# Optimization experiments

Measured on AMD Instinct MI355X. Metric: run time of the kernel, lower is better.

Reference implementation:

```python
import jax, jax.numpy as jnp
import numpy as np

T, N, NL, H, COND, NE, NSI, VOCAB = 32, 256, 16, 256, 64, 8, 16, 64


def _gru_step(h, x, wih, whh, bih, bhh):
    gi = x @ wih.T + bih
    gh = h @ whh.T + bhh
    ir, iz, inn = jnp.split(gi, 3, axis=-1)
    hr, hz, hn = jnp.split(gh, 3, axis=-1)
    r = jax.nn.sigmoid(ir + hr)
    z = jax.nn.sigmoid(iz + hz)
    n = jnp.tanh(inn + r * hn)
    return (1.0 - z) * n + z * h


def _run_gru(xs, wih, whh, bih, bhh, reverse=False):
    # xs: [B, L, D] -> [B, L, H]; zero initial state (torch default)
    def step(h, x):
        h = _gru_step(h, x, wih, whh, bih, bhh)
        return h, h
    h0 = jnp.zeros((xs.shape[0], whh.shape[1]), xs.dtype)
    _, ys = jax.lax.scan(step, h0, jnp.swapaxes(xs, 0, 1), reverse=reverse)
    return jnp.swapaxes(ys, 0, 1)


def _forward(condition, lines, actions, h0, w0, embed,
             gwih_f, gwhh_f, gbih_f, gbhh_f, gwih_b, gwhh_b, gbih_b, gbhh_b,
             w2, b2, cwih, cwhh, cbih, cbhh, mw1, mb1, mw2, mb2,
             ow, ob, aw, ab, cw, cb):
    M = embed[lines]                                   # [N, NL, H]
    # rolled[i] = roll(M, -i, axis=1); cat along batch dim -> [NL*N, NL, H]
    idx = (jnp.arange(NL)[:, None] + jnp.arange(NL)[None, :]) % NL
    rolled = jnp.transpose(M[:, idx], (1, 0, 2, 3)).reshape(NL * N, NL, H)
    yf = _run_gru(rolled, gwih_f, gwhh_f, gbih_f, gbhh_f)
    yb = _run_gru(rolled, gwih_b, gwhh_b, gbih_b, gbhh_b, reverse=True)
    G = jnp.stack([yf, yb], axis=2).reshape(NL, N, NL, 2, H)
    # pointer construction (no_scan=False branch)
    B = jax.nn.sigmoid(jnp.einsum('injdh,eh->injde', G, w2) + b2)  # [NL,N,NL,2,NE]
    f, b = B[..., 0, :], B[..., 1, :]
    Bc = jnp.stack([f, b[:, :, ::-1]], axis=3).reshape(NL, N, 2 * NL, NE)
    zero_last = Bc.at[:, :, -1].set(0.0)
    B2 = zero_last.at[:, :, -1].set(1.0)
    C = jnp.cumprod(1.0 - jnp.roll(zero_last, 1, axis=2), axis=2)
    P = (B2 * C).reshape(NL, N, NL, 2, NE)
    f2, b2p = P[..., 0, :], P[..., 1, :]
    P = jnp.concatenate([b2p[:, :, ::-1], f2], axis=2)  # [NL, N, 2NL, NE]
    P = jnp.roll(P, (-1, 1), axis=(0, 2))
    # per-timestep recurrence
    Rn = jnp.arange(N)
    A_seq = actions[:, :, 0]
    W_seq = actions[:, :, 1]

    def step(carry, xs):
        h, w = carry
        cond_t, A_t, W_t = xs
        x = jnp.concatenate([cond_t, M[Rn, w]], axis=-1)
        h = _gru_step(h, x, cwih, cwhh, cbih, cbhh)
        z = jax.nn.relu(jax.nn.relu(jax.nn.relu(h @ mw1.T + mb1) @ mw2.T + mb2))
        a_probs = jax.nn.softmax(z @ aw.T + ab)          # [N, NSI]
        o = jax.nn.softmax(z @ ow.T + ob)                # [N, NE]
        g = P[w, Rn]                                     # [N, 2NL, NE]
        p_probs = jnp.einsum('nke,ne->nk', g, o)         # [N, 2NL]
        v = z @ cw.T + cb                                # [N, 1]
        w_new = jnp.clip(w + W_t - NL, 0, NL - 1)
        fdt = z.dtype
        out = jnp.concatenate([
            A_t[:, None].astype(fdt), W_t[:, None].astype(fdt),
            w_new[:, None].astype(fdt), v, h, a_probs, p_probs], axis=-1)
        return (h, w_new), out

    _, ys = jax.lax.scan(step, (h0, w0), (condition, A_seq, W_seq))
    return ys  # [T, N, 4 + H + NSI + 2*NL]


def setup_inputs() -> dict:
    key = jax.random.key(0)
    ks = jax.random.split(key, 40)
    rn = lambda i, shape, s=0.05: (jax.random.normal(ks[i], shape) * s).astype(jnp.float32)
    H3 = 3 * H
    inp = {
        'condition': jax.random.normal(ks[0], (T, N, COND), jnp.float32),
        'lines': jax.random.randint(ks[1], (N, NL), 0, VOCAB, jnp.int32),
        'actions': jax.random.randint(ks[2], (T, N, 2), 0, 8, jnp.int32),
        'h0': jnp.zeros((N, H), jnp.float32),
        'w0': jnp.zeros((N,), jnp.int32),
        'embed': rn(3, (VOCAB, H), 0.5),
        'gwih_f': rn(4, (H3, H)), 'gwhh_f': rn(5, (H3, H)),
        'gbih_f': rn(6, (H3,)), 'gbhh_f': rn(7, (H3,)),
        'gwih_b': rn(8, (H3, H)), 'gwhh_b': rn(9, (H3, H)),
        'gbih_b': rn(10, (H3,)), 'gbhh_b': rn(11, (H3,)),
        'w2': rn(12, (NE, H)), 'b2': rn(13, (NE,)),
        'cwih': rn(14, (H3, H + COND)), 'cwhh': rn(15, (H3, H)),
        'cbih': rn(16, (H3,)), 'cbhh': rn(17, (H3,)),
        'mw1': rn(18, (H, H)), 'mb1': rn(19, (H,)),
        'mw2': rn(20, (H, H)), 'mb2': rn(21, (H,)),
        'ow': rn(22, (NE, H)), 'ob': rn(23, (NE,)),
        'aw': rn(24, (NSI, H)), 'ab': rn(25, (NSI,)),
        'cw': rn(26, (1, H)), 'cb': rn(27, (1,)),
    }
    return inp


def reference(condition, lines, actions, h0, w0, embed,
              gwih_f, gwhh_f, gbih_f, gbhh_f, gwih_b, gwhh_b, gbih_b, gbhh_b,
              w2, b2, cwih, cwhh, cbih, cbhh, mw1, mb1, mw2, mb2,
              ow, ob, aw, ab, cw, cb):
    return _forward(condition, lines, actions, h0, w0, embed,
                    gwih_f, gwhh_f, gbih_f, gbhh_f, gwih_b, gwhh_b, gbih_b, gbhh_b,
                    w2, b2, cwih, cwhh, cbih, cbhh, mw1, mb1, mw2, mb2,
                    ow, ob, aw, ab, cw, cb)
```

## Files before the change

### kernel.cpp

```cpp
#include <hip/hip_runtime.h>
#include <cstddef>
#include <cstdint>

#define TT   32
#define NN   256
#define NLL  16
#define HH   256
#define CONDD 64
#define NEE  8
#define H3   768
#define OW   308

typedef __attribute__((ext_vector_type(8))) short bf16x8;
typedef __attribute__((ext_vector_type(4))) float f32x4;
typedef unsigned short u16;

__device__ __forceinline__ float sigm(float x)     { return 1.f / (1.f + __expf(-x)); }
__device__ __forceinline__ float tanhfast(float x) { return 1.f - 2.f / (__expf(2.f * x) + 1.f); }
__device__ __forceinline__ float bf2f(u16 h) {
    union { unsigned u; float f; } v; v.u = ((unsigned)h) << 16; return v.f;
}
__device__ __forceinline__ u16 f2bf(float f) {
    union { float f; unsigned u; } v; v.f = f;
    unsigned r = v.u + 0x7fffu + ((v.u >> 16) & 1u);
    return (u16)(r >> 16);
}
#define MFMA(a, b, c) __builtin_amdgcn_mfma_f32_16x16x32_bf16(a, b, c, 0, 0, 0)

__device__ __forceinline__ void gl_lds16(const u16* g, u16* l) {
    __builtin_amdgcn_global_load_lds(
        (const __attribute__((address_space(1))) unsigned int*)(const void*)g,
        (__attribute__((address_space(3))) unsigned int*)(void*)l, 16, 0, 0);
}
__device__ __forceinline__ void stage_chunk(const u16* __restrict__ W, u16* buf,
                                            int c, int w, int lane) {
#pragma unroll
    for (int r = 0; r < 8; ++r) {
        int gran = (w * 8 + r) * 64 + lane;
        int cic = gran >> 5, gs = gran & 31;
        const u16* src = W + ((size_t)(c * 128 + cic) << 8) + ((gs ^ (cic & 7)) << 3);
        gl_lds16(src, buf + ((w * 8 + r) << 9));
    }
}
__device__ __forceinline__ void wait_vm8()   { asm volatile("s_waitcnt vmcnt(8)" ::: "memory"); }
__device__ __forceinline__ void wait_vm0()   { asm volatile("s_waitcnt vmcnt(0)" ::: "memory"); }
__device__ __forceinline__ void wait_lgkm0() { asm volatile("s_waitcnt lgkmcnt(0)" ::: "memory"); }
__device__ __forceinline__ void bar() {
    asm volatile("" ::: "memory");
    __builtin_amdgcn_s_barrier();
    asm volatile("" ::: "memory");
}

__global__ __launch_bounds__(256) void k_prep(
    const float* __restrict__ gwhh_f, const float* __restrict__ gwhh_b,
    const float* __restrict__ cwhh,  const float* __restrict__ mw1,
    const float* __restrict__ mw2,   const float* __restrict__ condition,
    const float* __restrict__ cwih,
    u16* __restrict__ whhbf_f, u16* __restrict__ whhbf_b, u16* __restrict__ cwhhbf,
    u16* __restrict__ mw1bf, u16* __restrict__ mw2bf, u16* __restrict__ condbf,
    u16* __restrict__ cwcbf)
{
    long i = (long)blockIdx.x * 256 + threadIdx.x;
    if (i < 196608) { whhbf_f[i] = f2bf(gwhh_f[i]); return; } i -= 196608;
    if (i < 196608) { whhbf_b[i] = f2bf(gwhh_b[i]); return; } i -= 196608;
    if (i < 196608) { cwhhbf[i]  = f2bf(cwhh[i]);  return; } i -= 196608;
    if (i < 65536)  { mw1bf[i]   = f2bf(mw1[i]);   return; } i -= 65536;
    if (i < 65536)  { mw2bf[i]   = f2bf(mw2[i]);   return; } i -= 65536;
    if (i < 524288) { condbf[i]  = f2bf(condition[i]); return; } i -= 524288;
    if (i < 49152)  { long r = i >> 6, c = i & 63; cwcbf[i] = f2bf(cwih[r * 320 + c]); }
}

__global__ __launch_bounds__(256) void k_tok_gi(
    const float* __restrict__ embed,
    const float* __restrict__ gwih_f, const float* __restrict__ gbih_f,
    const float* __restrict__ gwih_b, const float* __restrict__ gbih_b,
    const float* __restrict__ cwih,   const float* __restrict__ cbih,
    u16* __restrict__ gif, u16* __restrict__ gib, u16* __restrict__ gic)
{
    int v = blockIdx.x, tid = threadIdx.x;
    __shared__ float es[256];
    es[tid] = embed[v * HH + tid];
    __syncthreads();
    for (int g = 0; g < 3; ++g) {
        int col = g * 256 + tid;
        float af = gbih_f[col], abv = gbih_b[col], ac = cbih[col];
        const float* wf = gwih_f + (size_t)col * HH;
        const float* wb = gwih_b + (size_t)col * HH;
        const float* wc = cwih   + (size_t)col * (HH + CONDD) + CONDD;
        for (int c = 0; c < 256; ++c) {
            float e = es[c];
            af += e * wf[c]; abv += e * wb[c]; ac += e * wc[c];
        }
        gif[v * H3 + col] = f2bf(af);
        gib[v * H3 + col] = f2bf(abv);
        gic[v * H3 + col] = f2bf(ac);
    }
}

__global__ void k_wtraj(const int* __restrict__ actions, const int* __restrict__ w0,
                        const int* __restrict__ lines,
                        float* __restrict__ out, int* __restrict__ w_used,
                        int* __restrict__ tok_used)
{
    int n = threadIdx.x;
    int w = w0[n];
    for (int t = 0; t < TT; ++t) {
        int A = actions[((size_t)t * NN + n) * 2 + 0];
        int W = actions[((size_t)t * NN + n) * 2 + 1];
        w_used[t * NN + n] = w;
        tok_used[t * NN + n] = lines[n * NLL + w];
        int wn = w + W - NLL;
        wn = wn < 0 ? 0 : (wn > NLL - 1 ? NLL - 1 : wn);
        float* o = out + ((size_t)t * NN + n) * OW;
        o[0] = (float)A; o[1] = (float)W; o[2] = (float)wn;
        w = wn;
    }
}

__global__ __launch_bounds__(512) void k_gru(
    const u16* __restrict__ whhbf_f, const u16* __restrict__ whhbf_b,
    const u16* __restrict__ gif, const u16* __restrict__ gib,
    const float* __restrict__ gbhh_f, const float* __restrict__ gbhh_b,
    const float* __restrict__ w2, const float* __restrict__ b2,
    float* __restrict__ Bf, float* __restrict__ Bb,
    const int* __restrict__ lines)
{
    __shared__ __align__(16) u16 hbf[32 * 264];
    __shared__ __align__(16) u16 wbuf[2][32768];
    __shared__ float w2s[8 * 256];
    __shared__ int   lns[32 * 16];

    const int tid = threadIdx.x, lane = tid & 63, w = tid >> 6;
    const int lm = lane & 15, lg = lane >> 4;
    const int bid = blockIdx.x, dir = bid >> 7, lb = bid & 127;
    const int ii = lb >> 3, nb = (lb & 7) * 32;
    const u16*   whh  = dir ? whhbf_b : whhbf_f;
    const u16*   git  = dir ? gib : gif;
    const float* bhh  = dir ? gbhh_b : gbhh_f;
    float*       Bout = dir ? Bb : Bf;

    const int cicw = w * 16 + lm;
    const int cc0 = cicw, cc1 = cicw + 128;
    const float b_r[2] = { bhh[cc0],       bhh[cc1] };
    const float b_z[2] = { bhh[cc0 + 256], bhh[cc1 + 256] };
    const float b_n[2] = { bhh[cc0 + 512], bhh[cc1 + 512] };
    const float b2e = b2[tid & 7];

    for (int k = tid; k < 32 * 264; k += 512) hbf[k] = 0;
    for (int k = tid; k < 2048; k += 512) w2s[k] = w2[k];
    lns[tid & 511] = lines[(nb + (tid >> 4)) * NLL + (tid & 15)];
    __syncthreads();

    stage_chunk(whh, wbuf[0], 0, w, lane);

    for (int s = 0; s < 16; ++s) {
        const int jpos = dir ? (15 - s) : s;
        const int jt = (ii + jpos) & 15;

        bf16x8 a[2][8];
        #pragma unroll
        for (int ks = 0; ks < 8; ++ks) {
            a[0][ks] = *(const bf16x8*)&hbf[lm * 264 + ks * 32 + lg * 8];
            a[1][ks] = *(const bf16x8*)&hbf[(16 + lm) * 264 + ks * 32 + lg * 8];
        }
        f32x4 acc[6][2];
        #pragma unroll
        for (int c = 0; c < 6; ++c)
            #pragma unroll
            for (int rf = 0; rf < 2; ++rf)
                #pragma unroll
                for (int z = 0; z < 4; ++z) acc[c][rf][z] = 0.f;

        #pragma unroll
        for (int c = 0; c < 6; ++c) {
            if (s == 15 && c == 5) { wait_vm0(); }
            else { stage_chunk(whh, wbuf[(c + 1) & 1], (c + 1) % 6, w, lane); wait_vm8(); }
            bar();
            const u16* wb = wbuf[c & 1];
            #pragma unroll
            for (int ks = 0; ks < 8; ++ks) {
                bf16x8 b = *(const bf16x8*)&wb[(size_t)cicw * 256 + (((ks * 4 + lg) ^ (lm & 7)) << 3)];
                acc[c][0] = MFMA(a[0][ks], b, acc[c][0]);
                acc[c][1] = MFMA(a[1][ks], b, acc[c][1]);
            }
            bar();
        }

        float hnew[2][2][4];
        #pragma unroll
        for (int half = 0; half < 2; ++half) {
            const int cc = half ? cc1 : cc0;
            #pragma unroll
            for (int rf = 0; rf < 2; ++rf)
                #pragma unroll
                for (int j = 0; j < 4; ++j) {
                    int lrow = rf * 16 + lg * 4 + j;
                    int tok  = lns[lrow * 16 + jt];
                    const u16* gi = git + (size_t)tok * H3;
                    float ho = bf2f(hbf[lrow * 264 + cc]);
                    float rg = sigm(bf2f(gi[cc])       + acc[half][rf][j]     + b_r[half]);
                    float zg = sigm(bf2f(gi[cc + 256]) + acc[2 + half][rf][j] + b_z[half]);
                    float ng = tanhfast(bf2f(gi[cc + 512]) + rg * (acc[4 + half][rf][j] + b_n[half]));
                    hnew[half][rf][j] = (1.f - zg) * ng + zg * ho;
                }
        }
        #pragma unroll
        for (int half = 0; half < 2; ++half) {
            const int cc = half ? cc1 : cc0;
            #pragma unroll
            for (int rf = 0; rf < 2; ++rf)
                #pragma unroll
                for (int j = 0; j < 4; ++j)
                    hbf[(rf * 16 + lg * 4 + j) * 264 + cc] = f2bf(hnew[half][rf][j]);
        }
        wait_lgkm0(); bar();

        if (tid < 256) {
            int r = tid >> 3, e = tid & 7;
            float acb = b2e;
            for (int cx = 0; cx < 256; ++cx)
                acb += bf2f(hbf[r * 264 + cx]) * w2s[e * 256 + cx];
            int grow = ii * 256 + nb + r;
            Bout[((size_t)grow * NLL + jpos) * NEE + e] = sigm(acb);
        }
    }
}

__global__ __launch_bounds__(512) void k_ctrl(
    const u16* __restrict__ cwhhbf, const u16* __restrict__ cwcbf,
    const u16* __restrict__ condbf, const u16* __restrict__ gic,
    const float* __restrict__ cbhh, const float* __restrict__ h0,
    const int* __restrict__ tok_used,
    u16* __restrict__ Hallbf, float* __restrict__ out)
{
    __shared__ __align__(16) u16 hc[16 * 264];
    __shared__ __align__(16) u16 wbuf[2][32768];
    __shared__ int toks[16];

    const int tid = threadIdx.x, lane = tid & 63, w = tid >> 6;
    const int lm = lane & 15, lg = lane >> 4;
    const int cb = blockIdx.x;
    const int cicw = w * 16 + lm;
    const int cc0 = cicw, cc1 = cicw + 128;

    bf16x8 wc[6][2];
    #pragma unroll
    for (int c = 0; c < 6; ++c)
        #pragma unroll
        for (int k2 = 0; k2 < 2; ++k2)
            wc[c][k2] = *(const bf16x8*)&cwcbf[(size_t)(c * 128 + cicw) * 64 + k2 * 32 + lg * 8];

    const float cb_r[2] = { cbhh[cc0],       cbhh[cc1] };
    const float cb_z[2] = { cbhh[cc0 + 256], cbhh[cc1 + 256] };
    const float cb_n[2] = { cbhh[cc0 + 512], cbhh[cc1 + 512] };

    if (tid < 256) {
        int lrow = tid >> 4, c0 = (tid & 15) * 16;
        u16 tmp[16];
        #pragma unroll
        for (int k = 0; k < 16; ++k)
            tmp[k] = f2bf(h0[(size_t)(cb * 16 + lrow) * HH + c0 + k]);
        *(uint4*)&hc[lrow * 264 + c0]     = *(uint4*)&tmp[0];
        *(uint4*)&hc[lrow * 264 + c0 + 8] = *(uint4*)&tmp[8];
    }
    __syncthreads();

    stage_chunk(cwhhbf, wbuf[0], 0, w, lane);

    for (int t = 0; t < TT; ++t) {
        if (tid < 16) toks[tid] = tok_used[t * NN + cb * 16 + tid];

        bf16x8 a[8];
        #pragma unroll
        for (int ks = 0; ks < 8; ++ks)
            a[ks] = *(const bf16x8*)&hc[lm * 264 + ks * 32 + lg * 8];
        bf16x8 ca[2];
        #pragma unroll
        for (int k2 = 0; k2 < 2; ++k2)
            ca[k2] = *(const bf16x8*)&condbf[(size_t)(t * NN + cb * 16 + lm) * 64 + k2 * 32 + lg * 8];

        f32x4 acc[6], accC[2];
        #pragma unroll
        for (int c = 0; c < 6; ++c)
            #pragma unroll
            for (int z = 0; z < 4; ++z) acc[c][z] = 0.f;
        #pragma unroll
        for (int c = 0; c < 2; ++c)
            #pragma unroll
            for (int z = 0; z < 4; ++z) accC[c][z] = 0.f;

        #pragma unroll
        for (int c = 0; c < 6; ++c)
            #pragma unroll
            for (int k2 = 0; k2 < 2; ++k2) {
                if (c < 4) acc[c]      = MFMA(ca[k2], wc[c][k2], acc[c]);
                else       accC[c - 4] = MFMA(ca[k2], wc[c][k2], accC[c - 4]);
            }

        #pragma unroll
        for (int c = 0; c < 6; ++c) {
            if (t == 31 && c == 5) { wait_vm0(); }
            else { stage_chunk(cwhhbf, wbuf[(c + 1) & 1], (c + 1) % 6, w, lane); wait_vm8(); }
            bar();
            const u16* wb = wbuf[c & 1];
            #pragma unroll
            for (int ks = 0; ks < 8; ++ks) {
                bf16x8 b = *(const bf16x8*)&wb[(size_t)cicw * 256 + (((ks * 4 + lg) ^ (lm & 7)) << 3)];
                acc[c] = MFMA(a[ks], b, acc[c]);
            }
            bar();
        }

        float hn2[2][4];
        #pragma unroll
        for (int half = 0; half < 2; ++half) {
            const int cc = half ? cc1 : cc0;
            #pragma unroll
            for (int j = 0; j < 4; ++j) {
                int lrow = lg * 4 + j;
                int n = cb * 16 + lrow;
                int tok = toks[lrow];
                const u16* gi = gic + (size_t)tok * H3;
                float ho = bf2f(hc[lrow * 264 + cc]);
                float rg = sigm(bf2f(gi[cc])       + acc[half][j]     + cb_r[half]);
                float zg = sigm(bf2f(gi[cc + 256]) + acc[2 + half][j] + cb_z[half]);
                float ng = tanhfast(bf2f(gi[cc + 512]) + accC[half][j]
                                    + rg * (acc[4 + half][j] + cb_n[half]));
                float hn = (1.f - zg) * ng + zg * ho;
                out[((size_t)t * NN + n) * OW + 4 + cc] = hn;
                Hallbf[((size_t)t * NN + n) * HH + cc] = f2bf(hn);
                hn2[half][j] = hn;
            }
        }
        #pragma unroll
        for (int half = 0; half < 2; ++half) {
            const int cc = half ? cc1 : cc0;
            #pragma unroll
            for (int j = 0; j < 4; ++j)
                hc[(lg * 4 + j) * 264 + cc] = f2bf(hn2[half][j]);
        }
        wait_lgkm0(); bar();
    }
}

__global__ __launch_bounds__(256) void k_stick(
    const float* __restrict__ Bf, const float* __restrict__ Bb,
    float* __restrict__ P_final)
{
    int idx = blockIdx.x * 256 + threadIdx.x;
    if (idx >= 16 * 256 * 8) return;
    int e = idx & 7, n = (idx >> 3) & 255, i = idx >> 11;
    const float* bf = Bf + ((size_t)(i * NN + n) * NLL) * NEE + e;
    const float* bb = Bb + ((size_t)(i * NN + n) * NLL) * NEE + e;
    int i2 = (i + 15) & 15;
    float* dst = P_final + ((size_t)(i2 * NN + n) * 32) * NEE + e;
    float cum = 1.f;
    #pragma unroll
    for (int m = 0; m < 16; ++m) {
        float c0 = bf[m * NEE];
        float c1 = bb[(15 - m) * NEE];
        float v0 = c0 * cum;
        cum *= (1.f - c0);
        float v1 = (m < 15) ? c1 * cum : cum;
        cum *= (1.f - c1);
        dst[(size_t)(((17 + m) & 31)) * NEE] = v0;
        dst[(size_t)((16 - m)) * NEE]        = v1;
    }
}

__global__ __launch_bounds__(256) void k_mlp(
    const u16* __restrict__ A, const u16* __restrict__ W,
    const float* __restrict__ bias, u16* __restrict__ Out)
{
    __shared__ u16 ot[32 * 264];
    const int g0 = blockIdx.x * 32;
    const int tid = threadIdx.x, lane = tid & 63, w = tid >> 6;
    const int lm = lane & 15, lg = lane >> 4;
    f32x4 acc[4][2];
    #pragma unroll
    for (int c = 0; c < 4; ++c)
        #pragma unroll
        for (int r = 0; r < 2; ++r)
            #pragma unroll
            for (int z = 0; z < 4; ++z) acc[c][r][z] = 0.f;
    #pragma unroll
    for (int ks = 0; ks < 8; ++ks) {
        bf16x8 a0 = *(const bf16x8*)&A[(size_t)(g0 + lm) * 256 + ks * 32 + lg * 8];
        bf16x8 a1 = *(const bf16x8*)&A[(size_t)(g0 + 16 + lm) * 256 + ks * 32 + lg * 8];
        #pragma unroll
        for (int cf = 0; cf < 4; ++cf) {
            const u16* bp = W + (size_t)(w * 64 + cf * 16 + lm) * 256 + ks * 32 + lg * 8;
            bf16x8 b = *(const bf16x8*)bp;
            acc[cf][0] = MFMA(a0, b, acc[cf][0]);
            acc[cf][1] = MFMA(a1, b, acc[cf][1]);
        }
    }
    #pragma unroll
    for (int cf = 0; cf < 4; ++cf) {
        int col = w * 64 + cf * 16 + lm;
        float bs = bias[col];
        #pragma unroll
        for (int rf = 0; rf < 2; ++rf)
            #pragma unroll
            for (int j = 0; j < 4; ++j) {
                int lrow = rf * 16 + lg * 4 + j;
                ot[lrow * 264 + col] = f2bf(fmaxf(acc[cf][rf][j] + bs, 0.f));
            }
    }
    __syncthreads();
    int lrow = tid >> 3, c0 = (tid & 7) * 32;
    const uint4* src = (const uint4*)&ot[lrow * 264 + c0];
    uint4* dst = (uint4*)&Out[(size_t)(g0 + lrow) * 256 + c0];
    dst[0] = src[0]; dst[1] = src[1]; dst[2] = src[2]; dst[3] = src[3];
}

__global__ __launch_bounds__(256) void k_heads(
    const u16* __restrict__ zbf,
    const float* __restrict__ aw, const float* __restrict__ ab,
    const float* __restrict__ ow, const float* __restrict__ ob,
    const float* __restrict__ cw, const float* __restrict__ cb,
    const float* __restrict__ P_final, const int* __restrict__ w_used,
    float* __restrict__ out)
{
    __shared__ float zt[32 * 258];
    __shared__ float hd[32][28];
    __shared__ float o8[32][8];
    __shared__ int   wv[32];
    const int g0 = blockIdx.x * 32, tid = threadIdx.x;
    {
        int lrow = tid >> 3, c0 = (tid & 7) * 32;
        const u16* src = &zbf[(size_t)(g0 + lrow) * 256 + c0];
        #pragma unroll
        for (int k = 0; k < 32; ++k) zt[lrow * 258 + c0 + k] = bf2f(src[k]);
    }
    if (tid < 32) wv[tid] = w_used[g0 + tid];
    __syncthreads();
    {
        int r = tid >> 3, s = tid & 7;
        const float* z = &zt[r * 258];
        float a1 = ab[s], a2 = ab[8 + s], a3 = ob[s], a4 = cb[0];
        const float* w1 = aw + s * 256;
        const float* w2_ = aw + (8 + s) * 256;
        const float* w3 = ow + s * 256;
        for (int c = 0; c < 256; ++c) {
            float zv = z[c];
            a1 += zv * w1[c]; a2 += zv * w2_[c]; a3 += zv * w3[c]; a4 += zv * cw[c];
        }
        hd[r][s] = a1; hd[r][8 + s] = a2; hd[r][16 + s] = a3;
        if (s == 0) hd[r][24] = a4;
    }
    __syncthreads();
    if (tid < 32) {
        int r = tid; int g = g0 + r;
        float* orow = out + (size_t)g * OW;
        float mx = hd[r][0];
        #pragma unroll
        for (int k = 1; k < 16; ++k) mx = fmaxf(mx, hd[r][k]);
        float ex[16], ssum = 0.f;
        #pragma unroll
        for (int k = 0; k < 16; ++k) { ex[k] = __expf(hd[r][k] - mx); ssum += ex[k]; }
        float inv = 1.f / ssum;
        #pragma unroll
        for (int k = 0; k < 16; ++k) orow[260 + k] = ex[k] * inv;
        orow[3] = hd[r][24];
        float mo = hd[r][16];
        #pragma unroll
        for (int k = 1; k < 8; ++k) mo = fmaxf(mo, hd[r][16 + k]);
        float eo[8], so = 0.f;
        #pragma unroll
        for (int k = 0; k < 8; ++k) { eo[k] = __expf(hd[r][16 + k] - mo); so += eo[k]; }
        float invo = 1.f / so;
        #pragma unroll
        for (int k = 0; k < 8; ++k) o8[r][k] = eo[k] * invo;
    }
    __syncthreads();
    {
        int r = tid >> 3, kb = tid & 7;
        int g = g0 + r, n = g & 255;
        const float* base = P_final + ((size_t)(wv[r] * NN + n) * 32) * NEE;
        float* orow = out + (size_t)g * OW + 276;
        #pragma unroll
        for (int m = 0; m < 4; ++m) {
            int k = kb + m * 8;
            const float* pe = base + k * NEE;
            float a = 0.f;
            #pragma unroll
            for (int e = 0; e < 8; ++e) a += pe[e] * o8[r][e];
            orow[k] = a;
        }
    }
}

extern "C" void kernel_launch(void* const* d_in, const int* in_sizes, int n_in,
                              void* d_out, int out_size, void* d_ws, size_t ws_size,
                              hipStream_t stream) {
    const float* condition = (const float*)d_in[0];
    const int*   lines     = (const int*)  d_in[1];
    const int*   actions   = (const int*)  d_in[2];
    const float* h0        = (const float*)d_in[3];
    const int*   w0        = (const int*)  d_in[4];
    const float* embed     = (const float*)d_in[5];
    const float* gwih_f    = (const float*)d_in[6];
    const float* gwhh_f    = (const float*)d_in[7];
    const float* gbih_f    = (const float*)d_in[8];
    const float* gbhh_f    = (const float*)d_in[9];
    const float* gwih_b    = (const float*)d_in[10];
    const float* gwhh_b    = (const float*)d_in[11];
    const float* gbih_b    = (const float*)d_in[12];
    const float* gbhh_b    = (const float*)d_in[13];
    const float* w2        = (const float*)d_in[14];
    const float* b2        = (const float*)d_in[15];
    const float* cwih      = (const float*)d_in[16];
    const float* cwhh      = (const float*)d_in[17];
    const float* cbih      = (const float*)d_in[18];
    const float* cbhh      = (const float*)d_in[19];
    const float* mw1       = (const float*)d_in[20];
    const float* mb1       = (const float*)d_in[21];
    const float* mw2       = (const float*)d_in[22];
    const float* mb2       = (const float*)d_in[23];
    const float* ow        = (const float*)d_in[24];
    const float* ob        = (const float*)d_in[25];
    const float* aw        = (const float*)d_in[26];
    const float* ab        = (const float*)d_in[27];
    const float* cw        = (const float*)d_in[28];
    const float* cb        = (const float*)d_in[29];
    float* out = (float*)d_out;

    char* base = (char*)d_ws;
    auto alloc = [&](size_t bytes) { char* r = base; base += (bytes + 255) & ~(size_t)255; return r; };
    u16*   gif_tok = (u16*)alloc(64 * H3 * 2);
    u16*   gib_tok = (u16*)alloc(64 * H3 * 2);
    u16*   gic_tok = (u16*)alloc(64 * H3 * 2);
    u16*   whhbf_f = (u16*)alloc(H3 * 256 * 2);
    u16*   whhbf_b = (u16*)alloc(H3 * 256 * 2);
    u16*   cwhhbf  = (u16*)alloc(H3 * 256 * 2);
    u16*   mw1bf   = (u16*)alloc(256 * 256 * 2);
    u16*   mw2bf   = (u16*)alloc(256 * 256 * 2);
    u16*   cwcbf   = (u16*)alloc(H3 * 64 * 2);
    u16*   condbf  = (u16*)alloc((size_t)TT * NN * CONDD * 2);
    float* Bf      = (float*)alloc((size_t)16 * 256 * 16 * 8 * 4);
    float* Bb      = (float*)alloc((size_t)16 * 256 * 16 * 8 * 4);
    float* P_final = (float*)alloc((size_t)16 * 256 * 32 * 8 * 4);
    u16*   Hallbf  = (u16*)alloc((size_t)TT * NN * 256 * 2);
    u16*   zbf     = (u16*)alloc((size_t)TT * NN * 256 * 2);
    int*   w_used  = (int*)alloc((size_t)TT * NN * 4);
    int*   tok_used= (int*)alloc((size_t)TT * NN * 4);
    u16*   z1bf    = (u16*)Bf;

    k_prep<<<5056, 256, 0, stream>>>(gwhh_f, gwhh_b, cwhh, mw1, mw2, condition, cwih,
                                     whhbf_f, whhbf_b, cwhhbf, mw1bf, mw2bf, condbf, cwcbf);

    k_tok_gi<<<64, 256, 0, stream>>>(embed, gwih_f, gbih_f, gwih_b, gbih_b, cwih, cbih,
                                     gif_tok, gib_tok, gic_tok);
    k_wtraj<<<1, 256, 0, stream>>>(actions, w0, lines, out, w_used, tok_used);

    k_gru<<<256, 512, 0, stream>>>(whhbf_f, whhbf_b, gif_tok, gib_tok, gbhh_f, gbhh_b,
                                   w2, b2, Bf, Bb, lines);

    k_ctrl<<<16, 512, 0, stream>>>(cwhhbf, cwcbf, condbf, gic_tok, cbhh, h0, tok_used,
                                   Hallbf, out);

    k_stick<<<128, 256, 0, stream>>>(Bf, Bb, P_final);

    k_mlp<<<256, 256, 0, stream>>>(Hallbf, mw1bf, mb1, z1bf);
    k_mlp<<<256, 256, 0, stream>>>(z1bf, mw2bf, mb2, zbf);

    k_heads<<<256, 256, 0, stream>>>(zbf, aw, ab, ow, ob, cw, cb, P_final, w_used, out);
}
```

Before: 727.1 us.

## Merge pointer GRU and controller GRU into one concurrent kernel with 64-row tiles

Fuses the bidirectional pointer GRU and the controller GRU into a single launch. Blocks 0-127 run the pointer scans over 64 rows each, and blocks 128-131 run the controller over 64 rows each, so the long serial controller chain overlaps with the pointer work. The condition projection is precomputed for all timesteps by a new MFMA kernel into a gi_full buffer, and the token input projections and the r/z recurrent biases are folded together with MFMA. The w2 head now uses MFMA instead of a scalar loop, and hidden state is carried in fp32 registers. The costs are a large extra gi_full intermediate, buffer aliasing, and only 4 controller blocks, each doing a 32-step chain over more rows per step.

```diff
diff --git a/kernel.cpp b/kernel.cpp
--- a/kernel.cpp
+++ b/kernel.cpp
@@ -25,6 +25,12 @@
     unsigned r = v.u + 0x7fffu + ((v.u >> 16) & 1u);
     return (u16)(r >> 16);
 }
+__device__ __forceinline__ bf16x8 pack8(float4 f0, float4 f1) {
+    union { u16 u[8]; bf16x8 v; } r;
+    r.u[0] = f2bf(f0.x); r.u[1] = f2bf(f0.y); r.u[2] = f2bf(f0.z); r.u[3] = f2bf(f0.w);
+    r.u[4] = f2bf(f1.x); r.u[5] = f2bf(f1.y); r.u[6] = f2bf(f1.z); r.u[7] = f2bf(f1.w);
+    return r.v;
+}
 #define MFMA(a, b, c) __builtin_amdgcn_mfma_f32_16x16x32_bf16(a, b, c, 0, 0, 0)
 
 __device__ __forceinline__ void gl_lds16(const u16* g, u16* l) {
@@ -32,17 +38,17 @@
         (const __attribute__((address_space(1))) unsigned int*)(const void*)g,
         (__attribute__((address_space(3))) unsigned int*)(void*)l, 16, 0, 0);
 }
-__device__ __forceinline__ void stage_chunk(const u16* __restrict__ W, u16* buf,
-                                            int c, int w, int lane) {
+__device__ __forceinline__ void stage96(const u16* __restrict__ W, u16* buf,
+                                        int c, int w, int lane) {
 #pragma unroll
-    for (int r = 0; r < 8; ++r) {
-        int gran = (w * 8 + r) * 64 + lane;
-        int cic = gran >> 5, gs = gran & 31;
-        const u16* src = W + ((size_t)(c * 128 + cic) << 8) + ((gs ^ (cic & 7)) << 3);
-        gl_lds16(src, buf + ((w * 8 + r) << 9));
-    }
-}
-__device__ __forceinline__ void wait_vm8()   { asm volatile("s_waitcnt vmcnt(8)" ::: "memory"); }
+    for (int r = 0; r < 6; ++r) {
+        int gran = (w * 6 + r) * 64 + lane;
+        int row  = gran >> 5, gs = gran & 31;
+        const u16* src = W + ((size_t)(c * 96 + row) << 8) + ((gs ^ (row & 7)) << 3);
+        gl_lds16(src, buf + ((w * 6 + r) << 9));
+    }
+}
+__device__ __forceinline__ void wait_vm6()   { asm volatile("s_waitcnt vmcnt(6)" ::: "memory"); }
 __device__ __forceinline__ void wait_vm0()   { asm volatile("s_waitcnt vmcnt(0)" ::: "memory"); }
 __device__ __forceinline__ void wait_lgkm0() { asm volatile("s_waitcnt lgkmcnt(0)" ::: "memory"); }
 __device__ __forceinline__ void bar() {
@@ -54,10 +60,10 @@
 __global__ __launch_bounds__(256) void k_prep(
     const float* __restrict__ gwhh_f, const float* __restrict__ gwhh_b,
     const float* __restrict__ cwhh,  const float* __restrict__ mw1,
-    const float* __restrict__ mw2,   const float* __restrict__ condition,
+    const float* __restrict__ mw2,   const float* __restrict__ w2,
     const float* __restrict__ cwih,
     u16* __restrict__ whhbf_f, u16* __restrict__ whhbf_b, u16* __restrict__ cwhhbf,
-    u16* __restrict__ mw1bf, u16* __restrict__ mw2bf, u16* __restrict__ condbf,
+    u16* __restrict__ mw1bf, u16* __restrict__ mw2bf, u16* __restrict__ w2bf,
     u16* __restrict__ cwcbf)
 {
     long i = (long)blockIdx.x * 256 + threadIdx.x;
@@ -66,34 +72,58 @@
     if (i < 196608) { cwhhbf[i]  = f2bf(cwhh[i]);  return; } i -= 196608;
     if (i < 65536)  { mw1bf[i]   = f2bf(mw1[i]);   return; } i -= 65536;
     if (i < 65536)  { mw2bf[i]   = f2bf(mw2[i]);   return; } i -= 65536;
-    if (i < 524288) { condbf[i]  = f2bf(condition[i]); return; } i -= 524288;
+    if (i < 4096)   { long r = i >> 8, c = i & 255;
+                      w2bf[i] = (r < 8) ? f2bf(w2[r * 256 + c]) : (u16)0; return; } i -= 4096;
     if (i < 49152)  { long r = i >> 6, c = i & 63; cwcbf[i] = f2bf(cwih[r * 320 + c]); }
 }
 
-__global__ __launch_bounds__(256) void k_tok_gi(
+__global__ __launch_bounds__(256) void k_tok(
     const float* __restrict__ embed,
-    const float* __restrict__ gwih_f, const float* __restrict__ gbih_f,
-    const float* __restrict__ gwih_b, const float* __restrict__ gbih_b,
-    const float* __restrict__ cwih,   const float* __restrict__ cbih,
+    const float* __restrict__ gwih_f, const float* __restrict__ gbih_f, const float* __restrict__ gbhh_f,
+    const float* __restrict__ gwih_b, const float* __restrict__ gbih_b, const float* __restrict__ gbhh_b,
+    const float* __restrict__ cwih,   const float* __restrict__ cbih,   const float* __restrict__ cbhh,
     u16* __restrict__ gif, u16* __restrict__ gib, u16* __restrict__ gic)
 {
-    int v = blockIdx.x, tid = threadIdx.x;
-    __shared__ float es[256];
-    es[tid] = embed[v * HH + tid];
-    __syncthreads();
-    for (int g = 0; g < 3; ++g) {
-        int col = g * 256 + tid;
-        float af = gbih_f[col], abv = gbih_b[col], ac = cbih[col];
-        const float* wf = gwih_f + (size_t)col * HH;
-        const float* wb = gwih_b + (size_t)col * HH;
-        const float* wc = cwih   + (size_t)col * (HH + CONDD) + CONDD;
-        for (int c = 0; c < 256; ++c) {
-            float e = es[c];
-            af += e * wf[c]; abv += e * wb[c]; ac += e * wc[c];
-        }
-        gif[v * H3 + col] = f2bf(af);
-        gib[v * H3 + col] = f2bf(abv);
-        gic[v * H3 + col] = f2bf(ac);
+    const int mat = blockIdx.x / 6, ch = blockIdx.x % 6;
+    const int tid = threadIdx.x, lane = tid & 63, w = tid >> 6;
+    const int lm = lane & 15, lg = lane >> 4;
+    const float *W, *b1, *b2v; int wstride, woff; u16* dst;
+    if (mat == 0)      { W = gwih_f; b1 = gbih_f; b2v = gbhh_f; wstride = 256; woff = 0;  dst = gif; }
+    else if (mat == 1) { W = gwih_b; b1 = gbih_b; b2v = gbhh_b; wstride = 256; woff = 0;  dst = gib; }
+    else               { W = cwih;   b1 = cbih;   b2v = cbhh;   wstride = 320; woff = 64; dst = gic; }
+
+    bf16x8 a[8];
+    #pragma unroll
+    for (int ks = 0; ks < 8; ++ks) {
+        const float* ep = embed + (size_t)(w * 16 + lm) * 256 + ks * 32 + lg * 8;
+        a[ks] = pack8(*(const float4*)ep, *(const float4*)(ep + 4));
+    }
+    f32x4 acc[8];
+    #pragma unroll
+    for (int nt = 0; nt < 8; ++nt)
+        #pragma unroll
+        for (int z = 0; z < 4; ++z) acc[nt][z] = 0.f;
+
+    #pragma unroll
+    for (int nt = 0; nt < 8; ++nt) {
+        int col = ch * 128 + nt * 16 + lm;
+        const float* wp = W + (size_t)col * wstride + woff;
+        #pragma unroll
+        for (int ks = 0; ks < 8; ++ks) {
+            bf16x8 b = pack8(*(const float4*)(wp + ks * 32 + lg * 8),
+                             *(const float4*)(wp + ks * 32 + lg * 8 + 4));
+            acc[nt] = MFMA(a[ks], b, acc[nt]);
+        }
+    }
+    #pragma unroll
+    for (int nt = 0; nt < 8; ++nt) {
+        int col = ch * 128 + nt * 16 + lm;
+        float bias = b1[col] + (col < 512 ? b2v[col] : 0.f);
+        #pragma unroll
+        for (int j = 0; j < 4; ++j) {
+            int v = w * 16 + lg * 4 + j;
+            dst[(size_t)v * H3 + col] = f2bf(acc[nt][j] + bias);
+        }
     }
 }
 
@@ -117,229 +147,214 @@
     }
 }
 
-__global__ __launch_bounds__(512) void k_gru(
+__global__ __launch_bounds__(256) void k_cg(
+    const float* __restrict__ condition, const u16* __restrict__ cwcbf,
+    const u16* __restrict__ gic, const int* __restrict__ tok_used,
+    u16* __restrict__ gi_full)
+{
+    const int r0 = blockIdx.x * 32;
+    const int tid = threadIdx.x, lane = tid & 63, w = tid >> 6;
+    const int wm = w >> 1, wn = w & 1;
+    const int lm = lane & 15, lg = lane >> 4;
+
+    bf16x8 a[2];
+    #pragma unroll
+    for (int ks = 0; ks < 2; ++ks) {
+        const float* cp = condition + (size_t)(r0 + wm * 16 + lm) * 64 + ks * 32 + lg * 8;
+        a[ks] = pack8(*(const float4*)cp, *(const float4*)(cp + 4));
+    }
+    f32x4 acc[24];
+    #pragma unroll
+    for (int jj = 0; jj < 24; ++jj)
+        #pragma unroll
+        for (int z = 0; z < 4; ++z) acc[jj][z] = 0.f;
+
+    #pragma unroll
+    for (int jj = 0; jj < 24; ++jj) {
+        int tile = 2 * jj + wn;
+        const u16* bp = cwcbf + (size_t)(tile * 16 + lm) * 64;
+        #pragma unroll
+        for (int ks = 0; ks < 2; ++ks)
+            acc[jj] = MFMA(a[ks], *(const bf16x8*)(bp + ks * 32 + lg * 8), acc[jj]);
+    }
+    int wv[4];
+    #pragma unroll
+    for (int j = 0; j < 4; ++j) wv[j] = tok_used[r0 + wm * 16 + lg * 4 + j];
+    #pragma unroll
+    for (int jj = 0; jj < 24; ++jj) {
+        int col = (2 * jj + wn) * 16 + lm;
+        #pragma unroll
+        for (int j = 0; j < 4; ++j) {
+            int g = r0 + wm * 16 + lg * 4 + j;
+            float v = acc[jj][j] + bf2f(gic[(size_t)wv[j] * H3 + col]);
+            gi_full[(size_t)g * H3 + col] = f2bf(v);
+        }
+    }
+}
+
+__global__ __launch_bounds__(512) void k_mega(
     const u16* __restrict__ whhbf_f, const u16* __restrict__ whhbf_b,
+    const u16* __restrict__ cwhhbf,
     const u16* __restrict__ gif, const u16* __restrict__ gib,
     const float* __restrict__ gbhh_f, const float* __restrict__ gbhh_b,
-    const float* __restrict__ w2, const float* __restrict__ b2,
+    const float* __restrict__ cbhh,
+    const u16* __restrict__ w2bf, const float* __restrict__ b2,
     float* __restrict__ Bf, float* __restrict__ Bb,
-    const int* __restrict__ lines)
-{
-    __shared__ __align__(16) u16 hbf[32 * 264];
-    __shared__ __align__(16) u16 wbuf[2][32768];
-    __shared__ float w2s[8 * 256];
-    __shared__ int   lns[32 * 16];
+    const int* __restrict__ lines,
+    const u16* __restrict__ gi_full, const float* __restrict__ h0,
+    u16* __restrict__ Hallbf, float* __restrict__ out)
+{
+    __shared__ __align__(16) u16 hlds[64 * 264];
+    __shared__ __align__(16) u16 wbuf[2][96 * 256];
+    __shared__ __align__(16) u16 w2l[4096];
+    __shared__ int lns[1024];
 
     const int tid = threadIdx.x, lane = tid & 63, w = tid >> 6;
     const int lm = lane & 15, lg = lane >> 4;
-    const int bid = blockIdx.x, dir = bid >> 7, lb = bid & 127;
-    const int ii = lb >> 3, nb = (lb & 7) * 32;
-    const u16*   whh  = dir ? whhbf_b : whhbf_f;
-    const u16*   git  = dir ? gib : gif;
-    const float* bhh  = dir ? gbhh_b : gbhh_f;
-    float*       Bout = dir ? Bb : Bf;
-
-    const int cicw = w * 16 + lm;
-    const int cc0 = cicw, cc1 = cicw + 128;
-    const float b_r[2] = { bhh[cc0],       bhh[cc1] };
-    const float b_z[2] = { bhh[cc0 + 256], bhh[cc1 + 256] };
-    const float b_n[2] = { bhh[cc0 + 512], bhh[cc1 + 512] };
-    const float b2e = b2[tid & 7];
-
-    for (int k = tid; k < 32 * 264; k += 512) hbf[k] = 0;
-    for (int k = tid; k < 2048; k += 512) w2s[k] = w2[k];
-    lns[tid & 511] = lines[(nb + (tid >> 4)) * NLL + (tid & 15)];
+    const int wm = w >> 1, wn = w & 1;
+    const int bid = blockIdx.x;
+    const bool isctrl = (bid >= 128);
+
+    int dir = 0, ii = 0, nb = 0, cb = 0;
+    const u16* W; const u16* git = nullptr; const float* bnsrc;
+    float* Bout = nullptr;
+    if (isctrl) {
+        cb = bid - 128;
+        W = cwhhbf; bnsrc = cbhh;
+    } else {
+        dir = bid >> 6; int lb = bid & 63;
+        ii = lb >> 2; nb = (lb & 3) << 6;
+        W    = dir ? whhbf_b : whhbf_f;
+        git  = dir ? gib : gif;
+        bnsrc = dir ? gbhh_b : gbhh_f;
+        Bout = dir ? Bb : Bf;
+    }
+    const int smax = isctrl ? TT : 16;
+
+    float bn[8];
+    #pragma unroll
+    for (int jr = 0; jr < 8; ++jr) bn[jr] = bnsrc[512 + (2 * jr + wn) * 16 + lm];
+    const float b2e = (lm < 8) ? b2[lm] : 0.f;
+
+    float hreg[32];
+    if (isctrl) {
+        #pragma unroll
+        for (int jr = 0; jr < 8; ++jr) {
+            int col = (2 * jr + wn) * 16 + lm;
+            #pragma unroll
+            for (int j = 0; j < 4; ++j) {
+                int lrow = wm * 16 + lg * 4 + j;
+                float hv = h0[(size_t)(cb * 64 + lrow) * HH + col];
+                hreg[jr * 4 + j] = hv;
+                hlds[lrow * 264 + col] = f2bf(hv);
+            }
+        }
+    } else {
+        for (int k = tid; k < 64 * 264; k += 512) hlds[k] = 0;
+        #pragma unroll
+        for (int k = 0; k < 32; ++k) hreg[k] = 0.f;
+        for (int k = tid; k < 1024; k += 512)
+            lns[k] = lines[(nb + (k >> 4)) * NLL + (k & 15)];
+        for (int k = tid; k < 4096; k += 512) w2l[k] = w2bf[k];
+    }
     __syncthreads();
 
-    stage_chunk(whh, wbuf[0], 0, w, lane);
-
-    for (int s = 0; s < 16; ++s) {
-        const int jpos = dir ? (15 - s) : s;
-        const int jt = (ii + jpos) & 15;
-
-        bf16x8 a[2][8];
-        #pragma unroll
-        for (int ks = 0; ks < 8; ++ks) {
-            a[0][ks] = *(const bf16x8*)&hbf[lm * 264 + ks * 32 + lg * 8];
-            a[1][ks] = *(const bf16x8*)&hbf[(16 + lm) * 264 + ks * 32 + lg * 8];
-        }
-        f32x4 acc[6][2];
-        #pragma unroll
-        for (int c = 0; c < 6; ++c)
-            #pragma unroll
-            for (int rf = 0; rf < 2; ++rf)
-                #pragma unroll
-                for (int z = 0; z < 4; ++z) acc[c][rf][z] = 0.f;
-
-        #pragma unroll
-        for (int c = 0; c < 6; ++c) {
-            if (s == 15 && c == 5) { wait_vm0(); }
-            else { stage_chunk(whh, wbuf[(c + 1) & 1], (c + 1) % 6, w, lane); wait_vm8(); }
+    bf16x8 a[8];
+    #pragma unroll
+    for (int ks = 0; ks < 8; ++ks)
+        a[ks] = *(const bf16x8*)&hlds[(wm * 16 + lm) * 264 + ks * 32 + lg * 8];
+
+    stage96(W, wbuf[0], 0, w, lane);
+
+    for (int s = 0; s < smax; ++s) {
+        f32x4 acc[24];
+        #pragma unroll
+        for (int jj = 0; jj < 24; ++jj)
+            #pragma unroll
+            for (int z = 0; z < 4; ++z) acc[jj][z] = 0.f;
+
+        #pragma unroll
+        for (int c = 0; c < 8; ++c) {
+            if (c == 7 && s == smax - 1) { wait_vm0(); }
+            else { stage96(W, wbuf[(c + 1) & 1], (c + 1) & 7, w, lane); wait_vm6(); }
             bar();
             const u16* wb = wbuf[c & 1];
             #pragma unroll
-            for (int ks = 0; ks < 8; ++ks) {
-                bf16x8 b = *(const bf16x8*)&wb[(size_t)cicw * 256 + (((ks * 4 + lg) ^ (lm & 7)) << 3)];
-                acc[c][0] = MFMA(a[0][ks], b, acc[c][0]);
-                acc[c][1] = MFMA(a[1][ks], b, acc[c][1]);
+            for (int p = 0; p < 3; ++p) {
+                const int lt = wn + 2 * p;
+                const u16* bp = wb + ((lt * 16 + lm) << 8);
+                #pragma unroll
+                for (int ks = 0; ks < 8; ++ks) {
+                    bf16x8 b = *(const bf16x8*)(bp + (((ks * 4 + lg) ^ (lm & 7)) << 3));
+                    acc[c * 3 + p] = MFMA(a[ks], b, acc[c * 3 + p]);
+                }
             }
             bar();
         }
 
-        float hnew[2][2][4];
-        #pragma unroll
-        for (int half = 0; half < 2; ++half) {
-            const int cc = half ? cc1 : cc0;
-            #pragma unroll
-            for (int rf = 0; rf < 2; ++rf)
+        if (isctrl) {
+            #pragma unroll
+            for (int jr = 0; jr < 8; ++jr) {
+                const int col = (2 * jr + wn) * 16 + lm;
                 #pragma unroll
                 for (int j = 0; j < 4; ++j) {
-                    int lrow = rf * 16 + lg * 4 + j;
-                    int tok  = lns[lrow * 16 + jt];
+                    const int lrow = wm * 16 + lg * 4 + j;
+                    const size_t g = (size_t)s * NN + cb * 64 + lrow;
+                    const u16* gi = gi_full + g * H3;
+                    float rg = sigm(bf2f(gi[col])       + acc[jr][j]);
+                    float zg = sigm(bf2f(gi[col + 256]) + acc[8 + jr][j]);
+                    float ng = tanhfast(bf2f(gi[col + 512]) + rg * (acc[16 + jr][j] + bn[jr]));
+                    float hv = (1.f - zg) * ng + zg * hreg[jr * 4 + j];
+                    hreg[jr * 4 + j] = hv;
+                    hlds[lrow * 264 + col] = f2bf(hv);
+                    out[g * OW + 4 + col] = hv;
+                    Hallbf[g * HH + col] = f2bf(hv);
+                }
+            }
+        } else {
+            const int jpos = dir ? (15 - s) : s;
+            const int jt = (ii + jpos) & 15;
+            #pragma unroll
+            for (int jr = 0; jr < 8; ++jr) {
+                const int col = (2 * jr + wn) * 16 + lm;
+                #pragma unroll
+                for (int j = 0; j < 4; ++j) {
+                    const int lrow = wm * 16 + lg * 4 + j;
+                    const int tok = lns[lrow * 16 + jt];
                     const u16* gi = git + (size_t)tok * H3;
-                    float ho = bf2f(hbf[lrow * 264 + cc]);
-                    float rg = sigm(bf2f(gi[cc])       + acc[half][rf][j]     + b_r[half]);
-                    float zg = sigm(bf2f(gi[cc + 256]) + acc[2 + half][rf][j] + b_z[half]);
-                    float ng = tanhfast(bf2f(gi[cc + 512]) + rg * (acc[4 + half][rf][j] + b_n[half]));
-                    hnew[half][rf][j] = (1.f - zg) * ng + zg * ho;
+                    float rg = sigm(bf2f(gi[col])       + acc[jr][j]);
+                    float zg = sigm(bf2f(gi[col + 256]) + acc[8 + jr][j]);
+                    float ng = tanhfast(bf2f(gi[col + 512]) + rg * (acc[16 + jr][j] + bn[jr]));
+                    float hv = (1.f - zg) * ng + zg * hreg[jr * 4 + j];
+                    hreg[jr * 4 + j] = hv;
+                    hlds[lrow * 264 + col] = f2bf(hv);
                 }
-        }
-        #pragma unroll
-        for (int half = 0; half < 2; ++half) {
-            const int cc = half ? cc1 : cc0;
-            #pragma unroll
-            for (int rf = 0; rf < 2; ++rf)
+            }
+        }
+        wait_lgkm0(); bar();
+
+        #pragma unroll
+        for (int ks = 0; ks < 8; ++ks)
+            a[ks] = *(const bf16x8*)&hlds[(wm * 16 + lm) * 264 + ks * 32 + lg * 8];
+
+        if (!isctrl) {
+            const int jpos = dir ? (15 - s) : s;
+            f32x4 accB;
+            #pragma unroll
+            for (int z = 0; z < 4; ++z) accB[z] = 0.f;
+            #pragma unroll
+            for (int ks = 0; ks < 8; ++ks) {
+                bf16x8 wf = *(const bf16x8*)&w2l[lm * 256 + ks * 32 + lg * 8];
+                accB = MFMA(a[ks], wf, accB);
+            }
+            if (lm < 8) {
                 #pragma unroll
-                for (int j = 0; j < 4; ++j)
-                    hbf[(rf * 16 + lg * 4 + j) * 264 + cc] = f2bf(hnew[half][rf][j]);
-        }
-        wait_lgkm0(); bar();
-
-        if (tid < 256) {
-            int r = tid >> 3, e = tid & 7;
-            float acb = b2e;
-            for (int cx = 0; cx < 256; ++cx)
-                acb += bf2f(hbf[r * 264 + cx]) * w2s[e * 256 + cx];
-            int grow = ii * 256 + nb + r;
-            Bout[((size_t)grow * NLL + jpos) * NEE + e] = sigm(acb);
-        }
-    }
-}
-
-__global__ __launch_bounds__(512) void k_ctrl(
-    const u16* __restrict__ cwhhbf, const u16* __restrict__ cwcbf,
-    const u16* __restrict__ condbf, const u16* __restrict__ gic,
-    const float* __restrict__ cbhh, const float* __restrict__ h0,
-    const int* __restrict__ tok_used,
-    u16* __restrict__ Hallbf, float* __restrict__ out)
-{
-    __shared__ __align__(16) u16 hc[16 * 264];
-    __shared__ __align__(16) u16 wbuf[2][32768];
-    __shared__ int toks[16];
-
-    const int tid = threadIdx.x, lane = tid & 63, w = tid >> 6;
-    const int lm = lane & 15, lg = lane >> 4;
-    const int cb = blockIdx.x;
-    const int cicw = w * 16 + lm;
-    const int cc0 = cicw, cc1 = cicw + 128;
-
-    bf16x8 wc[6][2];
-    #pragma unroll
-    for (int c = 0; c < 6; ++c)
-        #pragma unroll
-        for (int k2 = 0; k2 < 2; ++k2)
-            wc[c][k2] = *(const bf16x8*)&cwcbf[(size_t)(c * 128 + cicw) * 64 + k2 * 32 + lg * 8];
-
-    const float cb_r[2] = { cbhh[cc0],       cbhh[cc1] };
-    const float cb_z[2] = { cbhh[cc0 + 256], cbhh[cc1 + 256] };
-    const float cb_n[2] = { cbhh[cc0 + 512], cbhh[cc1 + 512] };
-
-    if (tid < 256) {
-        int lrow = tid >> 4, c0 = (tid & 15) * 16;
-        u16 tmp[16];
-        #pragma unroll
-        for (int k = 0; k < 16; ++k)
-            tmp[k] = f2bf(h0[(size_t)(cb * 16 + lrow) * HH + c0 + k]);
-        *(uint4*)&hc[lrow * 264 + c0]     = *(uint4*)&tmp[0];
-        *(uint4*)&hc[lrow * 264 + c0 + 8] = *(uint4*)&tmp[8];
-    }
-    __syncthreads();
-
-    stage_chunk(cwhhbf, wbuf[0], 0, w, lane);
-
-    for (int t = 0; t < TT; ++t) {
-        if (tid < 16) toks[tid] = tok_used[t * NN + cb * 16 + tid];
-
-        bf16x8 a[8];
-        #pragma unroll
-        for (int ks = 0; ks < 8; ++ks)
-            a[ks] = *(const bf16x8*)&hc[lm * 264 + ks * 32 + lg * 8];
-        bf16x8 ca[2];
-        #pragma unroll
-        for (int k2 = 0; k2 < 2; ++k2)
-            ca[k2] = *(const bf16x8*)&condbf[(size_t)(t * NN + cb * 16 + lm) * 64 + k2 * 32 + lg * 8];
-
-        f32x4 acc[6], accC[2];
-        #pragma unroll
-        for (int c = 0; c < 6; ++c)
-            #pragma unroll
-            for (int z = 0; z < 4; ++z) acc[c][z] = 0.f;
-        #pragma unroll
-        for (int c = 0; c < 2; ++c)
-            #pragma unroll
-            for (int z = 0; z < 4; ++z) accC[c][z] = 0.f;
-
-        #pragma unroll
-        for (int c = 0; c < 6; ++c)
-            #pragma unroll
-            for (int k2 = 0; k2 < 2; ++k2) {
-                if (c < 4) acc[c]      = MFMA(ca[k2], wc[c][k2], acc[c]);
-                else       accC[c - 4] = MFMA(ca[k2], wc[c][k2], accC[c - 4]);
-            }
-
-        #pragma unroll
-        for (int c = 0; c < 6; ++c) {
-            if (t == 31 && c == 5) { wait_vm0(); }
-            else { stage_chunk(cwhhbf, wbuf[(c + 1) & 1], (c + 1) % 6, w, lane); wait_vm8(); }
-            bar();
-            const u16* wb = wbuf[c & 1];
-            #pragma unroll
-            for (int ks = 0; ks < 8; ++ks) {
-                bf16x8 b = *(const bf16x8*)&wb[(size_t)cicw * 256 + (((ks * 4 + lg) ^ (lm & 7)) << 3)];
-                acc[c] = MFMA(a[ks], b, acc[c]);
-            }
-            bar();
-        }
-
-        float hn2[2][4];
-        #pragma unroll
-        for (int half = 0; half < 2; ++half) {
-            const int cc = half ? cc1 : cc0;
-            #pragma unroll
-            for (int j = 0; j < 4; ++j) {
-                int lrow = lg * 4 + j;
-                int n = cb * 16 + lrow;
-                int tok = toks[lrow];
-                const u16* gi = gic + (size_t)tok * H3;
-                float ho = bf2f(hc[lrow * 264 + cc]);
-                float rg = sigm(bf2f(gi[cc])       + acc[half][j]     + cb_r[half]);
-                float zg = sigm(bf2f(gi[cc + 256]) + acc[2 + half][j] + cb_z[half]);
-                float ng = tanhfast(bf2f(gi[cc + 512]) + accC[half][j]
-                                    + rg * (acc[4 + half][j] + cb_n[half]));
-                float hn = (1.f - zg) * ng + zg * ho;
-                out[((size_t)t * NN + n) * OW + 4 + cc] = hn;
-                Hallbf[((size_t)t * NN + n) * HH + cc] = f2bf(hn);
-                hn2[half][j] = hn;
-            }
-        }
-        #pragma unroll
-        for (int half = 0; half < 2; ++half) {
-            const int cc = half ? cc1 : cc0;
-            #pragma unroll
-            for (int j = 0; j < 4; ++j)
-                hc[(lg * 4 + j) * 264 + cc] = f2bf(hn2[half][j]);
-        }
-        wait_lgkm0(); bar();
+                for (int j = 0; j < 4; ++j) {
+                    int nn = nb + wm * 16 + lg * 4 + j;
+                    Bout[(((size_t)ii * NN + nn) * NLL + jpos) * NEE + lm] = sigm(accB[j] + b2e);
+                }
+            }
+        }
     }
 }
 
@@ -536,29 +551,35 @@
     u16*   cwhhbf  = (u16*)alloc(H3 * 256 * 2);
     u16*   mw1bf   = (u16*)alloc(256 * 256 * 2);
     u16*   mw2bf   = (u16*)alloc(256 * 256 * 2);
+    u16*   w2bf    = (u16*)alloc(16 * 256 * 2);
     u16*   cwcbf   = (u16*)alloc(H3 * 64 * 2);
-    u16*   condbf  = (u16*)alloc((size_t)TT * NN * CONDD * 2);
+    u16*   gi_full = (u16*)alloc((size_t)TT * NN * H3 * 2);
     float* Bf      = (float*)alloc((size_t)16 * 256 * 16 * 8 * 4);
     float* Bb      = (float*)alloc((size_t)16 * 256 * 16 * 8 * 4);
-    float* P_final = (float*)alloc((size_t)16 * 256 * 32 * 8 * 4);
     u16*   Hallbf  = (u16*)alloc((size_t)TT * NN * 256 * 2);
-    u16*   zbf     = (u16*)alloc((size_t)TT * NN * 256 * 2);
     int*   w_used  = (int*)alloc((size_t)TT * NN * 4);
     int*   tok_used= (int*)alloc((size_t)TT * NN * 4);
+    float* P_final = (float*)gi_full;
+    u16*   zbf     = (u16*)((char*)gi_full + (size_t)4 * 1024 * 1024);
     u16*   z1bf    = (u16*)Bf;
 
-    k_prep<<<5056, 256, 0, stream>>>(gwhh_f, gwhh_b, cwhh, mw1, mw2, condition, cwih,
-                                     whhbf_f, whhbf_b, cwhhbf, mw1bf, mw2bf, condbf, cwcbf);
-
-    k_tok_gi<<<64, 256, 0, stream>>>(embed, gwih_f, gbih_f, gwih_b, gbih_b, cwih, cbih,
-                                     gif_tok, gib_tok, gic_tok);
+    k_prep<<<3024, 256, 0, stream>>>(gwhh_f, gwhh_b, cwhh, mw1, mw2, w2, cwih,
+                                     whhbf_f, whhbf_b, cwhhbf, mw1bf, mw2bf, w2bf, cwcbf);
+
+    k_tok<<<18, 256, 0, stream>>>(embed,
+                                  gwih_f, gbih_f, gbhh_f,
+                                  gwih_b, gbih_b, gbhh_b,
+                                  cwih, cbih, cbhh,
+                                  gif_tok, gib_tok, gic_tok);
+
     k_wtraj<<<1, 256, 0, stream>>>(actions, w0, lines, out, w_used, tok_used);
 
-    k_gru<<<256, 512, 0, stream>>>(whhbf_f, whhbf_b, gif_tok, gib_tok, gbhh_f, gbhh_b,
-                                   w2, b2, Bf, Bb, lines);
-
-    k_ctrl<<<16, 512, 0, stream>>>(cwhhbf, cwcbf, condbf, gic_tok, cbhh, h0, tok_used,
-                                   Hallbf, out);
+    k_cg<<<256, 256, 0, stream>>>(condition, cwcbf, gic_tok, tok_used, gi_full);
+
+    k_mega<<<132, 512, 0, stream>>>(whhbf_f, whhbf_b, cwhhbf,
+                                    gif_tok, gib_tok, gbhh_f, gbhh_b, cbhh,
+                                    w2bf, b2, Bf, Bb, lines,
+                                    gi_full, h0, Hallbf, out);
 
     k_stick<<<128, 256, 0, stream>>>(Bf, Bb, P_final);
 
```

Measured after the change: 1.411 ms. 94.0% more time.
